# Optimization experiments

Hardware: AMD Instinct MI355X
Metric: run time of the kernel (lower is better)

The kernel has to match this reference:

```python
import jax, jax.numpy as jnp
import numpy as np

N_NODES = 100000
N_EDGES = 1600000
C_IN = 64
C_OUT = 64


def setup_inputs() -> dict:
    key = jax.random.key(0)
    ks = jax.random.split(key, 8)
    x = jax.random.normal(ks[0], (N_NODES, C_IN), dtype=jnp.float32)
    edge_index = jax.random.randint(ks[1], (2, N_EDGES), 0, N_NODES, dtype=jnp.int64)
    s = 1.0 / np.sqrt(C_IN)
    # PyG SAGEConv(project=True) parameter layout
    lin_w = jax.random.uniform(ks[2], (C_IN, C_IN), jnp.float32, -s, s)   # lin: in->in
    lin_b = jax.random.uniform(ks[3], (C_IN,), jnp.float32, -s, s)
    linl_w = jax.random.uniform(ks[4], (C_OUT, C_IN), jnp.float32, -s, s)  # lin_l: in->out
    linl_b = jax.random.uniform(ks[5], (C_OUT,), jnp.float32, -s, s)
    linr_w = jax.random.uniform(ks[6], (C_OUT, C_IN), jnp.float32, -s, s)  # lin_r: in->out, no bias
    return {"x": x, "edge_index": edge_index, "lin_w": lin_w, "lin_b": lin_b,
            "linl_w": linl_w, "linl_b": linl_b, "linr_w": linr_w}


def reference(x, edge_index, lin_w, lin_b, linl_w, linl_b, linr_w):
    # x: (N, C_in); edge_index: (2, E) [src, dst]
    N = x.shape[0]
    src, dst = edge_index[0], edge_index[1]
    # gather neighbor features and project: lin(x[src])
    neigh = x[src] @ lin_w.T + lin_b                      # (E, C_in)
    # mean aggregation by destination node
    agg = jax.ops.segment_sum(neigh, dst, num_segments=N)  # (N, C_in)
    cnt = jax.ops.segment_sum(jnp.ones((dst.shape[0],), x.dtype), dst, num_segments=N)
    agg = agg / jnp.maximum(cnt, 1.0)[:, None]
    # out = lin_l(x) + lin_r(agg)
    return x @ linl_w.T + linl_b + agg @ linr_w.T
```

## Files before the change

### kernel.cpp

```cpp
#include <hip/hip_runtime.h>

#define C 64
#define NBLK 512
#define RN 256
#define CAP 6144

typedef __attribute__((ext_vector_type(8))) short bf16x8;
typedef __attribute__((ext_vector_type(4))) float f32x4;

__device__ __forceinline__ short f2bf(float f) {
    union { float f; unsigned u; } v; v.f = f;
    unsigned r = v.u + 0x7fff + ((v.u >> 16) & 1);
    return (short)(r >> 16);
}

__device__ __forceinline__ bf16x8 cvt8(const float* __restrict__ p, float scale) {
    bf16x8 r;
#pragma unroll
    for (int i = 0; i < 8; ++i) r[i] = f2bf(p[i] * scale);
    return r;
}

__global__ void precompute_wb(const float* __restrict__ lin_w,
                              const float* __restrict__ lin_b,
                              const float* __restrict__ linr_w,
                              float* __restrict__ Mrow,
                              float* __restrict__ bc) {
    int o = blockIdx.x;
    int j = threadIdx.x;
    float acc = 0.f;
#pragma unroll
    for (int i = 0; i < C; ++i)
        acc += linr_w[o * C + i] * lin_w[i * C + j];
    Mrow[o * C + j] = acc;
    if (j == 0) {
        float b = 0.f;
#pragma unroll
        for (int i = 0; i < C; ++i) b += linr_w[o * C + i] * lin_b[i];
        bc[o] = b;
    }
}

__global__ __launch_bounds__(256) void count_bins(const int* __restrict__ ei,
                                                  int* __restrict__ counts,
                                                  int E, int nsup) {
    __shared__ int bins[1024];
    int t = threadIdx.x, b = blockIdx.x;
    for (int i = t; i < nsup; i += 256) bins[i] = 0;
    __syncthreads();
    int epb = (E + NBLK - 1) / NBLK;
    int e0 = b * epb, e1 = min(E, e0 + epb);
    for (int e = e0 + t; e < e1; e += 256)
        atomicAdd(&bins[ei[E + e] >> 8], 1);
    __syncthreads();
    for (int i = t; i < nsup; i += 256) counts[i * NBLK + b] = bins[i];
}

__global__ __launch_bounds__(256) void sum_bins(const int* __restrict__ counts,
                                                int* __restrict__ rtot) {
    int r = blockIdx.x, t = threadIdx.x;
    const int* row = counts + (size_t)r * NBLK;
    int s = 0;
    for (int i = t; i < NBLK; i += 256) s += row[i];
    __shared__ int red[256];
    red[t] = s;
    __syncthreads();
    for (int o = 128; o > 0; o >>= 1) {
        if (t < o) red[t] += red[t + o];
        __syncthreads();
    }
    if (t == 0) rtot[r] = red[0];
}

__global__ __launch_bounds__(512) void scan_tot(const int* __restrict__ rtot,
                                                int* __restrict__ rstart, int nsup) {
    __shared__ int tmp[512];
    int t = threadIdx.x;
    int v = t < nsup ? rtot[t] : 0;
    tmp[t] = v;
    __syncthreads();
    for (int o = 1; o < 512; o <<= 1) {
        int u = (t >= o) ? tmp[t - o] : 0;
        __syncthreads();
        tmp[t] += u;
        __syncthreads();
    }
    if (t < nsup) rstart[t] = tmp[t] - v;
}

__global__ __launch_bounds__(512) void scan_bins(int* __restrict__ counts,
                                                 const int* __restrict__ rstart) {
    int r = blockIdx.x, t = threadIdx.x;
    int* row = counts + (size_t)r * NBLK;
    __shared__ int tmp[512];
    int v = t < NBLK ? row[t] : 0;
    tmp[t] = v;
    __syncthreads();
    for (int o = 1; o < 512; o <<= 1) {
        int u = (t >= o) ? tmp[t - o] : 0;
        __syncthreads();
        tmp[t] += u;
        __syncthreads();
    }
    if (t < NBLK) row[t] = rstart[r] + tmp[t] - v;
}

__global__ __launch_bounds__(256) void scatter_pairs(const int* __restrict__ ei,
                                                     const int* __restrict__ counts,
                                                     int* __restrict__ pairs,
                                                     int E, int nsup) {
    __shared__ int cur[1024];
    int t = threadIdx.x, b = blockIdx.x;
    for (int i = t; i < nsup; i += 256) cur[i] = counts[(size_t)i * NBLK + b];
    __syncthreads();
    int epb = (E + NBLK - 1) / NBLK;
    int e0 = b * epb, e1 = min(E, e0 + epb);
    for (int e = e0 + t; e < e1; e += 256) {
        int s = ei[e], d = ei[E + e];
        int pos = atomicAdd(&cur[d >> 8], 1);
        pairs[pos] = (s << 8) | (d & 255);
    }
}

__global__ __launch_bounds__(1024) void gather_fused(const float* __restrict__ x,
                                                     const int* __restrict__ pairs,
                                                     const int* __restrict__ rstart,
                                                     const int* __restrict__ rtot,
                                                     int* __restrict__ cnt,
                                                     float* __restrict__ agg, int N) {
    __shared__ int cntl[256], starts[256], cur[256], tmp[256];
    __shared__ int sorted[CAP];
    int t = threadIdx.x, r = blockIdx.x;
    int lo = r << 8;
    int base = rstart[r];
    int ne = min(rtot[r], CAP);

    if (t < 256) cntl[t] = 0;
    __syncthreads();
    for (int i = t; i < ne; i += 1024)
        atomicAdd(&cntl[pairs[base + i] & 255], 1);
    __syncthreads();
    if (t < 256) tmp[t] = cntl[t];
    __syncthreads();
    for (int o = 1; o < 256; o <<= 1) {
        int u = (t < 256 && t >= o) ? tmp[t - o] : 0;
        __syncthreads();
        if (t < 256) tmp[t] += u;
        __syncthreads();
    }
    if (t < 256) {
        starts[t] = tmp[t] - cntl[t];
        cur[t] = starts[t];
    }
    __syncthreads();
    for (int i = t; i < ne; i += 1024) {
        int p = pairs[base + i];
        int pos = atomicAdd(&cur[p & 255], 1);
        sorted[pos] = p >> 8;
    }
    __syncthreads();
    int wv = t >> 6, lane = t & 63, lg = lane >> 4, li = lane & 15;
    for (int l = wv; l < 256; l += 16) {
        int n = lo + l;
        if (n >= N) break;
        int s0 = starts[l], deg = cntl[l];
        float a[4] = {0, 0, 0, 0}, b2[4] = {0, 0, 0, 0};
        int i = 0;
        for (; i + 8 <= deg; i += 8) {
            int sA = sorted[s0 + i + lg];
            int sB = sorted[s0 + i + 4 + lg];
            float4 vA = *(const float4*)(x + (size_t)sA * C + (li << 2));
            float4 vB = *(const float4*)(x + (size_t)sB * C + (li << 2));
            a[0] += vA.x; a[1] += vA.y; a[2] += vA.z; a[3] += vA.w;
            b2[0] += vB.x; b2[1] += vB.y; b2[2] += vB.z; b2[3] += vB.w;
        }
        for (; i < deg; i += 4) {
            int idx = i + lg;
            int sA = sorted[s0 + min(idx, deg - 1)];
            float w = idx < deg ? 1.f : 0.f;
            float4 v = *(const float4*)(x + (size_t)sA * C + (li << 2));
            a[0] = fmaf(w, v.x, a[0]); a[1] = fmaf(w, v.y, a[1]);
            a[2] = fmaf(w, v.z, a[2]); a[3] = fmaf(w, v.w, a[3]);
        }
#pragma unroll
        for (int k = 0; k < 4; ++k) {
            a[k] += b2[k];
            a[k] += __shfl_xor(a[k], 16);
            a[k] += __shfl_xor(a[k], 32);
        }
        if (lane < 16) {
            float4 rr;
            rr.x = a[0]; rr.y = a[1]; rr.z = a[2]; rr.w = a[3];
            *(float4*)(agg + (size_t)n * C + (li << 2)) = rr;
        }
        if (lane == 0) cnt[n] = deg;
    }
}

__global__ __launch_bounds__(256) void matmul_mfma(const float* __restrict__ x,
                                                   const float* agg,
                                                   const int* __restrict__ cnt,
                                                   const float* __restrict__ linl_w,
                                                   const float* __restrict__ linl_b,
                                                   const float* __restrict__ Mrow,
                                                   const float* __restrict__ bc,
                                                   float* out, int N) {
    int t = threadIdx.x;
    int wv = t >> 6, lane = t & 63;
    int lrow = lane & 15;
    int kblk = lane >> 4;
    int koff = kblk * 8;

    bf16x8 Bf[4][4];
#pragma unroll
    for (int c = 0; c < 4; ++c) {
        int o = c * 16 + lrow;
#pragma unroll
        for (int q = 0; q < 4; ++q) {
            const float* src = (q < 2) ? (linl_w + (size_t)o * C + q * 32 + koff)
                                       : (Mrow + (size_t)o * C + (q - 2) * 32 + koff);
            Bf[c][q] = cvt8(src, 1.0f);
        }
    }
    float blv[4], bcv[4];
#pragma unroll
    for (int c = 0; c < 4; ++c) {
        blv[c] = linl_b[c * 16 + lrow];
        bcv[c] = bc[c * 16 + lrow];
    }

    int ntiles = (N + 15) >> 4;
    int nw = gridDim.x * 4;
    for (int tile = blockIdx.x * 4 + wv; tile < ntiles; tile += nw) {
        int n0 = tile * 16;
        int ar = min(n0 + lrow, N - 1);
        float inva = 1.0f / (float)max(cnt[ar], 1);
        const float* xr = x + (size_t)ar * C;
        const float* gr = agg + (size_t)ar * C;
        bf16x8 Af[4];
        Af[0] = cvt8(xr + koff, 1.0f);
        Af[1] = cvt8(xr + 32 + koff, 1.0f);
        Af[2] = cvt8(gr + koff, inva);
        Af[3] = cvt8(gr + 32 + koff, inva);

        f32x4 acc[4] = {{0, 0, 0, 0}, {0, 0, 0, 0}, {0, 0, 0, 0}, {0, 0, 0, 0}};
#pragma unroll
        for (int q = 0; q < 4; ++q)
#pragma unroll
            for (int c = 0; c < 4; ++c)
                acc[c] = __builtin_amdgcn_mfma_f32_16x16x32_bf16(Af[q], Bf[c][q],
                                                                 acc[c], 0, 0, 0);

#pragma unroll
        for (int r = 0; r < 4; ++r) {
            int nrow = n0 + kblk * 4 + r;
            if (nrow < N) {
                float ind = cnt[nrow] > 0 ? 1.f : 0.f;
#pragma unroll
                for (int c = 0; c < 4; ++c)
                    out[(size_t)nrow * C + c * 16 + lrow] =
                        acc[c][r] + blv[c] + ind * bcv[c];
            }
        }
    }
}

extern "C" void kernel_launch(void* const* d_in, const int* in_sizes, int n_in,
                              void* d_out, int out_size, void* d_ws, size_t ws_size,
                              hipStream_t stream) {
    const float* x      = (const float*)d_in[0];
    const int*   ei     = (const int*)d_in[1];
    const float* lin_w  = (const float*)d_in[2];
    const float* lin_b  = (const float*)d_in[3];
    const float* linl_w = (const float*)d_in[4];
    const float* linl_b = (const float*)d_in[5];
    const float* linr_w = (const float*)d_in[6];

    int N = in_sizes[0] / C;
    int E = in_sizes[1] / 2;
    int nsup = (N + RN - 1) / RN;

    int* counts = (int*)d_ws;
    int* rtot   = counts + (size_t)nsup * NBLK;
    int* rstart = rtot + nsup;
    int* cnt    = rstart + nsup;
    int* pairs  = cnt + N;
    float* Mrow = (float*)(pairs + E);
    float* bc   = Mrow + C * C;

    float* agg = (float*)d_out;

    precompute_wb<<<C, C, 0, stream>>>(lin_w, lin_b, linr_w, Mrow, bc);

    count_bins<<<NBLK, 256, 0, stream>>>(ei, counts, E, nsup);
    sum_bins<<<nsup, 256, 0, stream>>>(counts, rtot);
    scan_tot<<<1, 512, 0, stream>>>(rtot, rstart, nsup);
    scan_bins<<<nsup, 512, 0, stream>>>(counts, rstart);
    scatter_pairs<<<NBLK, 256, 0, stream>>>(ei, counts, pairs, E, nsup);

    gather_fused<<<nsup, 1024, 0, stream>>>(x, pairs, rstart, rtot, cnt, agg, N);

    int ntiles = (N + 15) / 16;
    int mblocks = (ntiles + 3) / 4;
    if (mblocks > 2048) mblocks = 2048;
    matmul_mfma<<<mblocks, 256, 0, stream>>>(x, agg, cnt, linl_w, linl_b, Mrow, bc,
                                             (float*)d_out, N);
}
```

Before: 212.1 us.

## Pre-convert x to bf16 and gather bf16 rows in aggregation

```diff
diff --git a/kernel.cpp b/kernel.cpp
--- a/kernel.cpp
+++ b/kernel.cpp
@@ -12,6 +12,12 @@
     union { float f; unsigned u; } v; v.f = f;
     unsigned r = v.u + 0x7fff + ((v.u >> 16) & 1);
     return (short)(r >> 16);
+}
+
+__device__ __forceinline__ float bf2f(short s) {
+    union { unsigned u; float f; } v;
+    v.u = ((unsigned)(unsigned short)s) << 16;
+    return v.f;
 }
 
 __device__ __forceinline__ bf16x8 cvt8(const float* __restrict__ p, float scale) {
@@ -41,6 +47,13 @@
     }
 }
 
+__global__ __launch_bounds__(256) void cvt_x(const float* __restrict__ x,
+                                             bf16x8* __restrict__ xb, int nchunk) {
+    int stride = gridDim.x * blockDim.x;
+    for (int i = blockIdx.x * blockDim.x + threadIdx.x; i < nchunk; i += stride)
+        xb[i] = cvt8(x + (size_t)i * 8, 1.0f);
+}
+
 __global__ __launch_bounds__(256) void count_bins(const int* __restrict__ ei,
                                                   int* __restrict__ counts,
                                                   int E, int nsup) {
@@ -122,7 +135,7 @@
     }
 }
 
-__global__ __launch_bounds__(1024) void gather_fused(const float* __restrict__ x,
+__global__ __launch_bounds__(1024) void gather_fused(const bf16x8* __restrict__ xb,
                                                      const int* __restrict__ pairs,
                                                      const int* __restrict__ rstart,
                                                      const int* __restrict__ rtot,
@@ -159,45 +172,55 @@
         sorted[pos] = p >> 8;
     }
     __syncthreads();
-    int wv = t >> 6, lane = t & 63, lg = lane >> 4, li = lane & 15;
+    int wv = t >> 6, lane = t & 63, g = lane >> 3, li2 = lane & 7;
     for (int l = wv; l < 256; l += 16) {
         int n = lo + l;
         if (n >= N) break;
         int s0 = starts[l], deg = cntl[l];
-        float a[4] = {0, 0, 0, 0}, b2[4] = {0, 0, 0, 0};
+        float a[8] = {0, 0, 0, 0, 0, 0, 0, 0}, b2[8] = {0, 0, 0, 0, 0, 0, 0, 0};
         int i = 0;
+        for (; i + 16 <= deg; i += 16) {
+            int sA = sorted[s0 + i + g];
+            int sB = sorted[s0 + i + 8 + g];
+            bf16x8 vA = xb[(size_t)sA * 8 + li2];
+            bf16x8 vB = xb[(size_t)sB * 8 + li2];
+#pragma unroll
+            for (int k = 0; k < 8; ++k) { a[k] += bf2f(vA[k]); b2[k] += bf2f(vB[k]); }
+        }
         for (; i + 8 <= deg; i += 8) {
-            int sA = sorted[s0 + i + lg];
-            int sB = sorted[s0 + i + 4 + lg];
-            float4 vA = *(const float4*)(x + (size_t)sA * C + (li << 2));
-            float4 vB = *(const float4*)(x + (size_t)sB * C + (li << 2));
-            a[0] += vA.x; a[1] += vA.y; a[2] += vA.z; a[3] += vA.w;
-            b2[0] += vB.x; b2[1] += vB.y; b2[2] += vB.z; b2[3] += vB.w;
-        }
-        for (; i < deg; i += 4) {
-            int idx = i + lg;
+            int sA = sorted[s0 + i + g];
+            bf16x8 vA = xb[(size_t)sA * 8 + li2];
+#pragma unroll
+            for (int k = 0; k < 8; ++k) a[k] += bf2f(vA[k]);
+        }
+        if (i < deg) {
+            int idx = i + g;
             int sA = sorted[s0 + min(idx, deg - 1)];
             float w = idx < deg ? 1.f : 0.f;
-            float4 v = *(const float4*)(x + (size_t)sA * C + (li << 2));
-            a[0] = fmaf(w, v.x, a[0]); a[1] = fmaf(w, v.y, a[1]);
-            a[2] = fmaf(w, v.z, a[2]); a[3] = fmaf(w, v.w, a[3]);
-        }
-#pragma unroll
-        for (int k = 0; k < 4; ++k) {
+            bf16x8 vA = xb[(size_t)sA * 8 + li2];
+#pragma unroll
+            for (int k = 0; k < 8; ++k) a[k] = fmaf(w, bf2f(vA[k]), a[k]);
+        }
+#pragma unroll
+        for (int k = 0; k < 8; ++k) {
             a[k] += b2[k];
+            a[k] += __shfl_xor(a[k], 8);
             a[k] += __shfl_xor(a[k], 16);
             a[k] += __shfl_xor(a[k], 32);
         }
-        if (lane < 16) {
-            float4 rr;
-            rr.x = a[0]; rr.y = a[1]; rr.z = a[2]; rr.w = a[3];
-            *(float4*)(agg + (size_t)n * C + (li << 2)) = rr;
+        if (g == 0) {
+            float4 r1, r2;
+            r1.x = a[0]; r1.y = a[1]; r1.z = a[2]; r1.w = a[3];
+            r2.x = a[4]; r2.y = a[5]; r2.z = a[6]; r2.w = a[7];
+            float* dst = agg + (size_t)n * C + li2 * 8;
+            *(float4*)dst = r1;
+            *(float4*)(dst + 4) = r2;
         }
         if (lane == 0) cnt[n] = deg;
     }
 }
 
-__global__ __launch_bounds__(256) void matmul_mfma(const float* __restrict__ x,
+__global__ __launch_bounds__(256) void matmul_mfma(const bf16x8* __restrict__ xb,
                                                    const float* agg,
                                                    const int* __restrict__ cnt,
                                                    const float* __restrict__ linl_w,
@@ -235,11 +258,10 @@
         int n0 = tile * 16;
         int ar = min(n0 + lrow, N - 1);
         float inva = 1.0f / (float)max(cnt[ar], 1);
-        const float* xr = x + (size_t)ar * C;
         const float* gr = agg + (size_t)ar * C;
         bf16x8 Af[4];
-        Af[0] = cvt8(xr + koff, 1.0f);
-        Af[1] = cvt8(xr + 32 + koff, 1.0f);
+        Af[0] = xb[(size_t)ar * 8 + kblk];
+        Af[1] = xb[(size_t)ar * 8 + 4 + kblk];
         Af[2] = cvt8(gr + koff, inva);
         Af[3] = cvt8(gr + 32 + koff, inva);
 
@@ -287,10 +309,14 @@
     int* pairs  = cnt + N;
     float* Mrow = (float*)(pairs + E);
     float* bc   = Mrow + C * C;
+    uintptr_t xaddr = ((uintptr_t)(bc + C) + 15) & ~(uintptr_t)15;
+    bf16x8* xb = (bf16x8*)xaddr;
 
     float* agg = (float*)d_out;
 
     precompute_wb<<<C, C, 0, stream>>>(lin_w, lin_b, linr_w, Mrow, bc);
+
+    cvt_x<<<2048, 256, 0, stream>>>(x, xb, N * 8);
 
     count_bins<<<NBLK, 256, 0, stream>>>(ei, counts, E, nsup);
     sum_bins<<<nsup, 256, 0, stream>>>(counts, rtot);
@@ -298,11 +324,11 @@
     scan_bins<<<nsup, 512, 0, stream>>>(counts, rstart);
     scatter_pairs<<<NBLK, 256, 0, stream>>>(ei, counts, pairs, E, nsup);
 
-    gather_fused<<<nsup, 1024, 0, stream>>>(x, pairs, rstart, rtot, cnt, agg, N);
+    gather_fused<<<nsup, 1024, 0, stream>>>(xb, pairs, rstart, rtot, cnt, agg, N);
 
     int ntiles = (N + 15) / 16;
     int mblocks = (ntiles + 3) / 4;
     if (mblocks > 2048) mblocks = 2048;
-    matmul_mfma<<<mblocks, 256, 0, stream>>>(x, agg, cnt, linl_w, linl_b, Mrow, bc,
+    matmul_mfma<<<mblocks, 256, 0, stream>>>(xb, agg, cnt, linl_w, linl_b, Mrow, bc,
                                              (float*)d_out, N);
 }
```

New measurement: 216.5 us. 2.1% more time.
